# Optimization experiments

Measured on AMD Instinct MI355X. Metric: run time of the kernel, lower is better.

The kernel has to match this reference:

```python
import jax, jax.numpy as jnp
import numpy as np

B, D, L = 16, 256, 200
T = 1000   # max_frame_length
K = 3      # kernel_size
DW, DC = 4, 2


def setup_inputs() -> dict:
    key = jax.random.key(0)
    ks = jax.random.split(key, 16)
    plen = jax.random.randint(ks[0], (B,), 150, L + 1)
    pm = jnp.arange(L)[None, :] < plen[:, None]              # (B,L) True=valid
    phoneme_mask = pm[:, None, :]                            # (B,1,L)
    durations = jax.random.uniform(ks[1], (B, L), minval=1.0, maxval=8.0) * pm
    phoneme = jax.random.normal(ks[2], (B, D, L), dtype=jnp.float32)
    s = 0.05
    params = {
        'Wpw': jax.random.normal(ks[3], (D, D)) * s, 'bpw': jnp.zeros((D,)),
        'Cw': jax.random.normal(ks[4], (8, D, K)) * s, 'cbw': jnp.zeros((8,)),
        'Mw': jax.random.normal(ks[5], (10, DW)) * s, 'mbw': jnp.zeros((DW,)),
        'Lw': jax.random.normal(ks[6], (DW * D, D)) * s, 'lbw': jnp.zeros((D,)),
        'Wpc': jax.random.normal(ks[7], (D, D)) * s, 'bpc': jnp.zeros((D,)),
        'Cc': jax.random.normal(ks[8], (8, D, K)) * s, 'cbc': jnp.zeros((8,)),
        'Mc': jax.random.normal(ks[9], (10, DC)) * s, 'mbc': jnp.zeros((DC,)),
        'Lc': jax.random.normal(ks[10], (DW * DC, D)) * s, 'lbc': jnp.zeros((D,)),
        'Wo': jax.random.normal(ks[11], (D, 2 * D)) * s, 'bo': jnp.zeros((2 * D,)),
    }
    return {'durations': durations, 'phoneme': phoneme, 'phoneme_mask': phoneme_mask, **params}


def _conv_swish(x, W1, b1, Ck, cb, pm):
    # 1x1 conv (proj) then kernel-K 'same' conv then SiLU; mask padded phones
    h = jnp.einsum('od,bdl->bol', W1, x) + b1[None, :, None]
    h = jax.lax.conv_general_dilated(h, Ck, (1,), 'SAME',
                                     dimension_numbers=('NCH', 'OIH', 'NCH')) + cb[None, :, None]
    h = jax.nn.silu(h)
    h = jnp.where(pm[:, None, :], h, 0.0)
    return h.transpose(0, 2, 1)  # (B, L, 8)


def _mlp(S, E, h, M, mb):
    # concat start/end boundary scalars with per-phone conv features -> (B,T,L,10)
    feat = jnp.concatenate([S[..., None], E[..., None],
                            jnp.broadcast_to(h[:, None], (B, T, L, 8))], axis=-1)
    return jax.nn.silu(feat @ M + mb)


def _forward(durations, phoneme, phoneme_mask, Wpw, bpw, Cw, cbw, Mw, mbw, Lw, lbw,
             Wpc, bpc, Cc, cbc, Mc, mbc, Lc, lbc, Wo, bo):
    pm = phoneme_mask[:, 0, :]                                          # (B,L)
    frame_lengths = jnp.clip(jnp.round(durations.sum(-1)).astype(jnp.int32), 0, T)
    frame_mask = jnp.arange(T)[None, :] < frame_lengths[:, None]        # (B,T)
    attn_mask = frame_mask[:, :, None] & pm[:, None, :]                 # (B,T,L)
    sd = jnp.cumsum(durations, axis=-1)                                 # (B,L)
    sk = sd - durations
    t = jnp.arange(1, T + 1, dtype=durations.dtype)
    S = jnp.where(attn_mask, t[None, :, None] - sk[:, None, :], 0.0)    # (B,T,L)
    E = jnp.where(attn_mask, (sd - sk)[:, None, :], 0.0)                # (B,T,L)

    h_w = _conv_swish(phoneme, Wpw, bpw, Cw, cbw, pm)
    w = _mlp(S, E, h_w, Mw, mbw)                                        # (B,T,L,DW)
    w = jnp.where(pm[:, None, :, None], w, -jnp.inf)
    w = jax.nn.softmax(w, axis=2)                                       # softmax over phones
    w = jnp.where(frame_mask[:, :, None, None], w, 0.0)

    h_c = _conv_swish(phoneme, Wpc, bpc, Cc, cbc, pm)
    c = _mlp(S, E, h_c, Mc, mbc)                                        # (B,T,L,DC)

    wh = jnp.einsum('btlq,bdl->btqd', w, phoneme).reshape(B, T, DW * D) @ Lw + lbw
    wc = jnp.einsum('btlq,btlp->btqp', w, c).reshape(B, T, DW * DC) @ Lc + lbc
    whc = jnp.where(frame_mask[..., None], wh + wc, 0.0)                # (B,T,D)
    out = (whc @ Wo + bo).transpose(0, 2, 1)                            # (B,2D,T)
    return out, frame_mask, frame_lengths, w.transpose(0, 3, 1, 2)


def reference(durations, phoneme, phoneme_mask, Wpw, bpw, Cw, cbw, Mw, mbw, Lw, lbw,
              Wpc, bpc, Cc, cbc, Mc, mbc, Lc, lbc, Wo, bo):
    out, frame_mask, frame_lengths, w = _forward(
        durations, phoneme, phoneme_mask, Wpw, bpw, Cw, cbw, Mw, mbw, Lw, lbw,
        Wpc, bpc, Cc, cbc, Mc, mbc, Lc, lbc, Wo, bo)
    mean, log_std = jnp.split(out, 2, axis=1)                           # (B,D,T) each
    return (mean, log_std, frame_mask, frame_lengths, w)
```

## Files before the change

kernel.cpp:

```cpp
#include <hip/hip_runtime.h>
#include <hip/hip_bf16.h>
#include <math.h>

#define NB 16
#define ND 256
#define NL 200
#define NT 1000

typedef unsigned short ushort_t;
typedef __bf16 bf16x8 __attribute__((ext_vector_type(8)));
typedef float f32x4 __attribute__((ext_vector_type(4)));

#define OFF_PHT   0u
#define OFF_WCS   1000000u
#define OFF_SK    4966400u
#define OFF_EW    4969600u
#define OFF_EC    4975744u
#define OFF_BW2   4981888u
#define OFF_BC2   4981912u
#define OFF_FL    4981936u
#define OFF_WG    4981952u
#define OFF_GT    11535552u
#define OFF_WOT   15221952u
#define OFF_BASE  15287488u
#define OFF_PHTB  15320256u
#define OFF_LWT   15844544u

__device__ __forceinline__ float silu_f(float x){ return x / (1.f + __expf(-x)); }
__device__ __forceinline__ ushort_t f2bf(float x){
  __hip_bfloat16 h = __float2bfloat16(x);
  return *(ushort_t*)&h;
}

__global__ __launch_bounds__(256) void k_stage1(
    const float* __restrict__ dur, const float* __restrict__ ph,
    const float* __restrict__ Wp_w, const float* __restrict__ C_w, const float* __restrict__ bp_w,
    const float* __restrict__ Wp_c, const float* __restrict__ C_c, const float* __restrict__ bp_c,
    const float* __restrict__ Wo, const float* __restrict__ Lw,
    float* __restrict__ sk_ws, int* __restrict__ fl_ws,
    float* __restrict__ o_fm, float* __restrict__ o_fl,
    float* __restrict__ Ew, float* __restrict__ Ec,
    float* __restrict__ bw2, float* __restrict__ bc2,
    ushort_t* __restrict__ WoT, ushort_t* __restrict__ LwT,
    float* __restrict__ phT, ushort_t* __restrict__ phTb)
{
  int bid = blockIdx.x, tid = threadIdx.x;
  if (bid < 16){
    int b = bid;
    __shared__ float sdur[NL];
    __shared__ float ssk[NL];
    __shared__ int sfl;
    if (tid < NL) sdur[tid] = dur[b*NL + tid];
    __syncthreads();
    if (tid == 0){
      float run = 0.f;
      for (int l = 0; l < NL; ++l){ ssk[l] = run; run += sdur[l]; }
      int fl = (int)rintf(run);
      fl = fl < 0 ? 0 : (fl > NT ? NT : fl);
      sfl = fl; fl_ws[b] = fl; o_fl[b] = (float)fl;
    }
    __syncthreads();
    if (tid < NL) sk_ws[b*NL + tid] = ssk[tid];
    for (int t = tid; t < NT; t += 256) o_fm[b*NT + t] = (t < sfl) ? 1.f : 0.f;
  } else if (bid < 1600){
    int sbid = bid - 16;
    if (sbid < 48){
      int gid = sbid*256 + tid;
      int branch = gid / 6144;
      int r = gid % 6144;
      int d = r & 255;
      int ock = r >> 8;
      int oc = ock / 3, k = ock % 3;
      const float* Wp = branch ? Wp_c : Wp_w;
      const float* C  = branch ? C_c  : C_w;
      float acc = 0.f;
      for (int i = 0; i < ND; ++i) acc += C[(oc*ND + i)*3 + k] * Wp[i*ND + d];
      (branch ? Ec : Ew)[r] = acc;
      if (d == 0){
        const float* bp = branch ? bp_c : bp_w;
        float bb = 0.f;
        for (int i = 0; i < ND; ++i) bb += C[(oc*ND + i)*3 + k] * bp[i];
        (branch ? bc2 : bw2)[ock] = bb;
      }
    } else {
      int gid = (sbid - 48)*256 + tid;
      if (gid < 131072){
        int n = gid >> 8, k = gid & 255;
        WoT[gid] = f2bf(Wo[(size_t)k*512 + n]);
      } else {
        int r = gid - 131072;
        int d = r & 255;
        int qn = r >> 8;
        int q = qn >> 8, n = qn & 255;
        LwT[r] = f2bf(Lw[((size_t)q*256 + d)*256 + n]);
      }
    }
  } else {
    int r = bid - 1600;
    int xb = r & 7, yb = (r >> 3) & 7, b = r >> 6;
    int l0 = xb*32, d0 = yb*32;
    int tx = tid & 31, ty = tid >> 5;
    __shared__ float tile[32][33];
    #pragma unroll
    for (int i = 0; i < 4; ++i){
      int d = d0 + ty + i*8, l = l0 + tx;
      tile[ty + i*8][tx] = (l < NL) ? ph[((size_t)b*ND + d)*NL + l] : 0.f;
    }
    __syncthreads();
    #pragma unroll
    for (int i = 0; i < 4; ++i){
      int l = l0 + ty + i*8, d = d0 + tx;
      float v = tile[tx][ty + i*8];
      if (l < NL) phT[((size_t)b*NL + l)*ND + d] = v;
      phTb[((size_t)b*256 + l)*ND + d] = f2bf(v);
    }
  }
}

__global__ __launch_bounds__(256) void k_stage2(
    const float* __restrict__ phT,
    const float* __restrict__ dur, const float* __restrict__ sk_ws,
    const float* __restrict__ Ew, const float* __restrict__ Ec,
    const float* __restrict__ bw2, const float* __restrict__ bc2,
    const float* __restrict__ cbw, const float* __restrict__ cbc,
    const float* __restrict__ Mw, const float* __restrict__ mbw,
    const float* __restrict__ Mc, const float* __restrict__ mbc,
    float4* __restrict__ base,
    const ushort_t* __restrict__ LwT, const ushort_t* __restrict__ phTb,
    ushort_t* __restrict__ Gt)
{
  __shared__ __align__(16) unsigned char smem[128*136*2];
  int bid = blockIdx.x, tid = threadIdx.x;
  if (bid < 256){
    int b = bid >> 4, x = bid & 15;
    if (x >= 13){
      int l0 = 208 + (x - 13)*16;
      if (tid < 32)
        base[((size_t)(b*256 + l0 + (tid >> 1)))*2 + (tid & 1)] = make_float4(0,0,0,0);
      return;
    }
    float (*sh)[17] = (float (*)[17])smem;
    int lu = tid >> 4, u = tid & 15;
    int l = x*16 + lu;
    float h = 0.f;
    if (l < NL){
      int branch = u >> 3, oc = u & 7;
      const float* E  = branch ? Ec  : Ew;
      const float* b2 = branch ? bc2 : bw2;
      float val = (branch ? cbc : cbw)[oc];
      #pragma unroll
      for (int k = 0; k < 3; ++k){
        int ll = l + k - 1;
        if (ll < 0 || ll >= NL) continue;
        float acc = b2[oc*3 + k];
        const float4* Er = (const float4*)(E + (oc*3 + k)*ND);
        const float4* pr = (const float4*)(phT + ((size_t)b*NL + ll)*ND);
        #pragma unroll 8
        for (int d = 0; d < 64; ++d){
          float4 e = Er[d], p = pr[d];
          acc += e.x*p.x + e.y*p.y + e.z*p.z + e.w*p.w;
        }
        val += acc;
      }
      float pm = (dur[b*NL + l] > 0.5f) ? 1.f : 0.f;
      h = silu_f(val) * pm;
    }
    sh[lu][u] = h;
    __syncthreads();
    if (tid < 16){
      int ll = x*16 + tid;
      float4 o0 = make_float4(0,0,0,0);
      float4 o1 = make_float4(0,0,0,0);
      if (ll < NL){
        float dl  = dur[b*NL + ll];
        float pm  = (dl > 0.5f) ? 1.f : 0.f;
        float skl = sk_ws[b*NL + ll];
        float c1[4], c2[2];
        #pragma unroll
        for (int q = 0; q < 4; ++q) c1[q] = mbw[q] + dl*Mw[4 + q] - skl*Mw[q];
        #pragma unroll
        for (int p = 0; p < 2; ++p) c2[p] = mbc[p] + dl*Mc[2 + p] - skl*Mc[p];
        #pragma unroll
        for (int j = 0; j < 8; ++j){
          float hwv = sh[tid][j], hcv = sh[tid][8 + j];
          #pragma unroll
          for (int q = 0; q < 4; ++q) c1[q] += hwv*Mw[(2 + j)*4 + q];
          #pragma unroll
          for (int p = 0; p < 2; ++p) c2[p] += hcv*Mc[(2 + j)*2 + p];
        }
        o0 = make_float4(c1[0], c1[1], c1[2], c1[3]);
        o1 = make_float4(c2[0], c2[1], pm, 0.f);
      }
      base[((size_t)(b*256 + ll))*2 + 0] = o0;
      base[((size_t)(b*256 + ll))*2 + 1] = o1;
    }
  } else {
    int r = bid - 256;
    int xb = r & 1, yb = (r >> 1) & 1, bq = r >> 2;
    int b = bq >> 2, q = bq & 3;
    int m0 = yb * 128;
    int n0 = xb * 128;
    int lane = tid & 63, wave = tid >> 6;
    int wm = wave >> 1, wn = wave & 1;
    int col = lane & 15, kg4 = lane >> 4;
    f32x4 acc[4][4] = {};
    for (int kt = 0; kt < 8; ++kt){
      int k0 = kt*32;
      bf16x8 afr[4], bfr[4];
      #pragma unroll
      for (int i = 0; i < 4; ++i)
        afr[i] = *(const bf16x8*)(LwT + ((size_t)(q*256 + m0 + wm*64 + i*16 + col))*256 + k0 + kg4*8);
      #pragma unroll
      for (int j = 0; j < 4; ++j)
        bfr[j] = *(const bf16x8*)(phTb + ((size_t)(b*256 + n0 + wn*64 + j*16 + col))*256 + k0 + kg4*8);
      #pragma unroll
      for (int i = 0; i < 4; ++i)
        #pragma unroll
        for (int j = 0; j < 4; ++j)
          acc[i][j] = __builtin_amdgcn_mfma_f32_16x16x32_bf16(afr[i], bfr[j], acc[i][j], 0, 0, 0);
    }
    ushort_t (*st2)[136] = (ushort_t (*)[136])smem;
    int rq = lane >> 4;
    #pragma unroll
    for (int i = 0; i < 4; ++i){
      #pragma unroll
      for (int rr = 0; rr < 4; ++rr){
        int rl = wm*64 + i*16 + rq*4 + rr;
        #pragma unroll
        for (int j = 0; j < 4; ++j){
          int cl = wn*64 + j*16 + col;
          st2[rl][cl] = f2bf(acc[i][j][rr]);
        }
      }
    }
    __syncthreads();
    #pragma unroll
    for (int rep = 0; rep < 8; ++rep){
      int row = rep*16 + (tid >> 4);
      int ch  = tid & 15;
      int l   = n0 + ch*8;
      if (l < NL){
        int n = m0 + row;
        *(uint4*)(Gt + ((size_t)(b*ND + n))*800 + q*NL + l) = *(const uint4*)&st2[row][ch*8];
      }
    }
  }
}

__global__ __launch_bounds__(256) void k_softmax(
    const float4* __restrict__ base,
    const int* __restrict__ fl_ws,
    const float* __restrict__ Mw, const float* __restrict__ Mc,
    float* __restrict__ wout,
    ushort_t* __restrict__ wG,
    float* __restrict__ wcs_g)
{
  int lane = threadIdx.x & 63, wave = threadIdx.x >> 6;
  int wid = blockIdx.x*4 + wave;
  int b = wid >> 10, t = wid & 1023;
  int fl = fl_ws[b];
  ushort_t* wrow = wG + ((size_t)(b << 10) + t)*800;

  if (t >= fl){
    uint4 z16; z16.x = z16.y = z16.z = z16.w = 0u;
    for (int k = lane; k < 100; k += 64)
      *(uint4*)&wrow[k*8] = z16;
    if (lane < 8) wcs_g[((size_t)(b << 10) + t)*8 + lane] = 0.f;
    if (t < NT && lane < 50){
      float4 z4 = make_float4(0,0,0,0);
      #pragma unroll
      for (int q = 0; q < 4; ++q)
        *(float4*)&wout[(((size_t)(b*4 + q))*NT + t)*NL + lane*4] = z4;
    }
    return;
  }

  int l0 = lane*4;
  bool lv = (l0 < NL);
  float b0a[4][4], b1x[4], b1y[4], pmv[4];
  #pragma unroll
  for (int e = 0; e < 4; ++e){
    float4 v0 = make_float4(0,0,0,0), v1 = make_float4(0,0,0,0);
    if (lv){
      v0 = base[((size_t)(b*256 + l0 + e))*2 + 0];
      v1 = base[((size_t)(b*256 + l0 + e))*2 + 1];
    }
    b0a[e][0] = v0.x; b0a[e][1] = v0.y; b0a[e][2] = v0.z; b0a[e][3] = v0.w;
    b1x[e] = v1.x; b1y[e] = v1.y; pmv[e] = v1.z;
  }
  float tf = (float)(t + 1);

  float z[4][4], mx[4] = {-INFINITY, -INFINITY, -INFINITY, -INFINITY};
  #pragma unroll
  for (int e = 0; e < 4; ++e){
    #pragma unroll
    for (int q = 0; q < 4; ++q){
      float sv = silu_f(b0a[e][q] + tf*Mw[q]);
      float zv = (pmv[e] > 0.f) ? sv : -INFINITY;
      z[e][q] = zv;
      mx[q] = fmaxf(mx[q], zv);
    }
  }
  #pragma unroll
  for (int q = 0; q < 4; ++q){
    float v = mx[q];
    #pragma unroll
    for (int off = 32; off; off >>= 1) v = fmaxf(v, __shfl_xor(v, off));
    mx[q] = v;
  }
  float s4[4] = {0,0,0,0};
  #pragma unroll
  for (int e = 0; e < 4; ++e){
    #pragma unroll
    for (int q = 0; q < 4; ++q){
      float ev = (pmv[e] > 0.f) ? __expf(z[e][q] - mx[q]) : 0.f;
      z[e][q] = ev;
      s4[q] += ev;
    }
  }
  #pragma unroll
  for (int q = 0; q < 4; ++q){
    float v = s4[q];
    #pragma unroll
    for (int off = 32; off; off >>= 1) v += __shfl_xor(v, off);
    s4[q] = 1.f / v;
  }
  float cv[4][2];
  #pragma unroll
  for (int e = 0; e < 4; ++e){
    cv[e][0] = silu_f(b1x[e] + tf*Mc[0]);
    cv[e][1] = silu_f(b1y[e] + tf*Mc[1]);
  }
  float wc[8] = {0,0,0,0,0,0,0,0};
  #pragma unroll
  for (int q = 0; q < 4; ++q){
    float w0 = z[0][q]*s4[q];
    float w1 = z[1][q]*s4[q];
    float w2 = z[2][q]*s4[q];
    float w3 = z[3][q]*s4[q];
    if (lv){
      *(float4*)&wout[(((size_t)(b*4 + q))*NT + t)*NL + l0] =
          make_float4(w0, w1, w2, w3);
      uint2 pk;
      pk.x = (unsigned)f2bf(w0) | ((unsigned)f2bf(w1) << 16);
      pk.y = (unsigned)f2bf(w2) | ((unsigned)f2bf(w3) << 16);
      *(uint2*)&wrow[q*NL + l0] = pk;
    }
    wc[q*2 + 0] += w0*cv[0][0] + w1*cv[1][0] + w2*cv[2][0] + w3*cv[3][0];
    wc[q*2 + 1] += w0*cv[0][1] + w1*cv[1][1] + w2*cv[2][1] + w3*cv[3][1];
  }
  #pragma unroll
  for (int x = 0; x < 8; ++x){
    float v = wc[x];
    #pragma unroll
    for (int off = 32; off; off >>= 1) v += __shfl_xor(v, off);
    wc[x] = v;
  }
  if (lane == 0){
    #pragma unroll
    for (int x = 0; x < 8; ++x) wcs_g[((size_t)(b << 10) + t)*8 + x] = wc[x];
  }
}

#define TT 64
__global__ __launch_bounds__(1024, 4) void k_wv2(
    const int* __restrict__ fl_ws,
    const ushort_t* __restrict__ wG,
    const ushort_t* __restrict__ Gt,
    const float* __restrict__ wcs_g,
    const float* __restrict__ Lc,
    const float* __restrict__ lbc,
    const float* __restrict__ lbw,
    const ushort_t* __restrict__ WoT,
    const float* __restrict__ bo,
    float* __restrict__ o_mean, float* __restrict__ o_lstd)
{
  __shared__ ushort_t stc[TT][264];
  __shared__ float wcs_l[TT][8];
  int b = blockIdx.x;
  int m0 = blockIdx.y * TT;
  int tid = threadIdx.x, lane = tid & 63, wave = tid >> 6;
  int col = lane & 15, kg4 = lane >> 4;
  int fl = fl_ws[b];

  if (fl <= m0){
    for (int idx = tid; idx < 512*16; idx += 1024){
      int s = idx >> 4, j = idx & 15;
      int t0 = m0 + j*4;
      if (t0 + 3 < NT){
        float v = bo[s];
        float4 v4 = make_float4(v, v, v, v);
        if (s < ND) *(float4*)&o_mean[((size_t)b*ND + s)*NT + t0] = v4;
        else        *(float4*)&o_lstd[((size_t)b*ND + (s - ND))*NT + t0] = v4;
      }
    }
    return;
  }

  if (tid < 512){
    int tl = tid >> 3, u = tid & 7;
    wcs_l[tl][u] = wcs_g[((size_t)(b << 10) + m0 + tl)*8 + u];
  }

  f32x4 acc[4] = {};
  const ushort_t* Gb = Gt + (size_t)b*ND*800;
  const ushort_t* Wb = wG + ((size_t)(b << 10) + m0)*800;
  for (int kt = 0; kt < 25; ++kt){
    int k0 = kt*32;
    bf16x8 afr[4], bfr;
    #pragma unroll
    for (int i = 0; i < 4; ++i)
      afr[i] = *(const bf16x8*)(Wb + ((size_t)(i*16 + col))*800 + k0 + kg4*8);
    bfr = *(const bf16x8*)(Gb + ((size_t)(wave*16 + col))*800 + k0 + kg4*8);
    #pragma unroll
    for (int i = 0; i < 4; ++i)
      acc[i] = __builtin_amdgcn_mfma_f32_16x16x32_bf16(afr[i], bfr, acc[i], 0, 0, 0);
  }
  __syncthreads();

  {
    int rq = lane >> 4;
    int n = wave*16 + col;
    float lbn = lbc[n], lbwn = lbw[n];
    float lcn[8];
    #pragma unroll
    for (int u = 0; u < 8; ++u) lcn[u] = Lc[u*ND + n];
    #pragma unroll
    for (int i = 0; i < 4; ++i){
      #pragma unroll
      for (int r = 0; r < 4; ++r){
        int tl = i*16 + rq*4 + r;
        int t = m0 + tl;
        if (t < NT){
          float f = (t < fl) ? 1.f : 0.f;
          float vcv = lbn
            + wcs_l[tl][0]*lcn[0] + wcs_l[tl][1]*lcn[1]
            + wcs_l[tl][2]*lcn[2] + wcs_l[tl][3]*lcn[3]
            + wcs_l[tl][4]*lcn[4] + wcs_l[tl][5]*lcn[5]
            + wcs_l[tl][6]*lcn[6] + wcs_l[tl][7]*lcn[7];
          stc[tl][n] = f2bf(f * (acc[i][r] + lbwn + vcv));
        }
      }
    }
  }
  __syncthreads();

  {
    f32x4 acc2[2][4] = {};
    for (int kt = 0; kt < 8; ++kt){
      int k0 = kt*32;
      bf16x8 afr[2], bfr[4];
      #pragma unroll
      for (int j = 0; j < 4; ++j)
        bfr[j] = *(const bf16x8*)(&stc[j*16 + col][k0 + kg4*8]);
      #pragma unroll
      for (int i = 0; i < 2; ++i)
        afr[i] = *(const bf16x8*)(WoT + ((size_t)(wave*32 + i*16 + col))*ND + k0 + kg4*8);
      #pragma unroll
      for (int i = 0; i < 2; ++i)
        #pragma unroll
        for (int j = 0; j < 4; ++j)
          acc2[i][j] = __builtin_amdgcn_mfma_f32_16x16x32_bf16(afr[i], bfr[j], acc2[i][j], 0, 0, 0);
    }
    int rq = lane >> 4;
    #pragma unroll
    for (int i = 0; i < 2; ++i){
      #pragma unroll
      for (int r = 0; r < 4; ++r){
        int s = wave*32 + i*16 + rq*4 + r;
        float bov = bo[s];
        #pragma unroll
        for (int j = 0; j < 4; ++j){
          int t = m0 + j*16 + col;
          if (t < NT){
            float v = acc2[i][j][r] + bov;
            if (s < ND) o_mean[((size_t)b*ND + s)*NT + t] = v;
            else        o_lstd[((size_t)b*ND + (s - ND))*NT + t] = v;
          }
        }
      }
    }
  }
}

extern "C" void kernel_launch(void* const* d_in, const int* in_sizes, int n_in,
                              void* d_out, int out_size, void* d_ws, size_t ws_size,
                              hipStream_t stream)
{
  const float* dur = (const float*)d_in[0];
  const float* ph  = (const float*)d_in[1];
  const float* Wpw = (const float*)d_in[3];
  const float* bpw = (const float*)d_in[4];
  const float* Cw  = (const float*)d_in[5];
  const float* cbw = (const float*)d_in[6];
  const float* Mw  = (const float*)d_in[7];
  const float* mbw = (const float*)d_in[8];
  const float* Lw  = (const float*)d_in[9];
  const float* lbw = (const float*)d_in[10];
  const float* Wpc = (const float*)d_in[11];
  const float* bpc = (const float*)d_in[12];
  const float* Cc  = (const float*)d_in[13];
  const float* cbc = (const float*)d_in[14];
  const float* Mc  = (const float*)d_in[15];
  const float* mbc = (const float*)d_in[16];
  const float* Lc  = (const float*)d_in[17];
  const float* lbc = (const float*)d_in[18];
  const float* Wo  = (const float*)d_in[19];
  const float* bo  = (const float*)d_in[20];

  float* out    = (float*)d_out;
  float* o_mean = out;
  float* o_lstd = out + (size_t)NB*ND*NT;
  float* o_fm   = o_lstd + (size_t)NB*ND*NT;
  float* o_fl   = o_fm + NB*NT;
  float* o_w    = o_fl + NB;

  float* ws   = (float*)d_ws;
  float* phT  = ws + OFF_PHT;
  float* wcsg = ws + OFF_WCS;
  float* sk   = ws + OFF_SK;
  float* Ew   = ws + OFF_EW;
  float* Ec   = ws + OFF_EC;
  float* bw2  = ws + OFF_BW2;
  float* bc2  = ws + OFF_BC2;
  int*   fl   = (int*)(ws + OFF_FL);
  ushort_t* wG   = (ushort_t*)(ws + OFF_WG);
  ushort_t* Gt   = (ushort_t*)(ws + OFF_GT);
  ushort_t* WoT  = (ushort_t*)(ws + OFF_WOT);
  float4*   base = (float4*)(ws + OFF_BASE);
  ushort_t* phTb = (ushort_t*)(ws + OFF_PHTB);
  ushort_t* LwT  = (ushort_t*)(ws + OFF_LWT);

  k_stage1<<<2624, 256, 0, stream>>>(dur, ph, Wpw, Cw, bpw, Wpc, Cc, bpc, Wo, Lw,
                                     sk, fl, o_fm, o_fl, Ew, Ec, bw2, bc2,
                                     WoT, LwT, phT, phTb);
  k_stage2<<<512, 256, 0, stream>>>(phT, dur, sk, Ew, Ec, bw2, bc2, cbw, cbc,
                                    Mw, mbw, Mc, mbc, base, LwT, phTb, Gt);
  k_softmax<<<4096, 256, 0, stream>>>(base, fl, Mw, Mc, o_w, wG, wcsg);
  {
    dim3 g(NB, 16);
    k_wv2<<<g, 1024, 0, stream>>>(fl, wG, Gt, wcsg, Lc, lbc, lbw,
                                  WoT, bo, o_mean, o_lstd);
  }
}
```

Measured before the change: 260.2 us.

## Fuse softmax attention weights into the weighted-value GEMM kernel via LDS

New measurement: 250.9 us. -3.6%, faster.

```diff
diff --git a/kernel.cpp b/kernel.cpp
--- a/kernel.cpp
+++ b/kernel.cpp
@@ -12,14 +12,12 @@
 typedef float f32x4 __attribute__((ext_vector_type(4)));
 
 #define OFF_PHT   0u
-#define OFF_WCS   1000000u
 #define OFF_SK    4966400u
 #define OFF_EW    4969600u
 #define OFF_EC    4975744u
 #define OFF_BW2   4981888u
 #define OFF_BC2   4981912u
 #define OFF_FL    4981936u
-#define OFF_WG    4981952u
 #define OFF_GT    11535552u
 #define OFF_WOT   15221952u
 #define OFF_BASE  15287488u
@@ -247,36 +245,71 @@
   }
 }
 
-__global__ __launch_bounds__(256) void k_softmax(
+#define AP 808
+#define TT 48
+__global__ __launch_bounds__(512, 4) void k_wv_fused(
     const float4* __restrict__ base,
     const int* __restrict__ fl_ws,
     const float* __restrict__ Mw, const float* __restrict__ Mc,
+    const ushort_t* __restrict__ Gt,
+    const float* __restrict__ Lc,
+    const float* __restrict__ lbc,
+    const float* __restrict__ lbw,
+    const ushort_t* __restrict__ WoT,
+    const float* __restrict__ bo,
     float* __restrict__ wout,
-    ushort_t* __restrict__ wG,
-    float* __restrict__ wcs_g)
+    float* __restrict__ o_mean, float* __restrict__ o_lstd)
 {
-  int lane = threadIdx.x & 63, wave = threadIdx.x >> 6;
-  int wid = blockIdx.x*4 + wave;
-  int b = wid >> 10, t = wid & 1023;
+  __shared__ ushort_t As[TT*AP];
+  __shared__ float    wcs[TT][8];
+  int b = blockIdx.x;
+  int m0 = blockIdx.y * TT;
+  int tid = threadIdx.x, lane = tid & 63, wave = tid >> 6;
+  int col = lane & 15, kg4 = lane >> 4;
   int fl = fl_ws[b];
-  ushort_t* wrow = wG + ((size_t)(b << 10) + t)*800;
-
-  if (t >= fl){
-    uint4 z16; z16.x = z16.y = z16.z = z16.w = 0u;
-    for (int k = lane; k < 100; k += 64)
-      *(uint4*)&wrow[k*8] = z16;
-    if (lane < 8) wcs_g[((size_t)(b << 10) + t)*8 + lane] = 0.f;
-    if (t < NT && lane < 50){
-      float4 z4 = make_float4(0,0,0,0);
-      #pragma unroll
-      for (int q = 0; q < 4; ++q)
-        *(float4*)&wout[(((size_t)(b*4 + q))*NT + t)*NL + lane*4] = z4;
+
+  if (fl <= m0){
+    for (int idx = tid; idx < TT*4*50; idx += 512){
+      int tl = idx / 200;
+      int rqs = idx - tl*200;
+      int q = rqs / 50, seg = rqs - q*50;
+      int t = m0 + tl;
+      if (t < NT)
+        *(float4*)&wout[(((size_t)(b*4 + q))*NT + t)*NL + seg*4] = make_float4(0,0,0,0);
+    }
+    for (int idx = tid; idx < 512*12; idx += 512){
+      int s = idx / 12, j = idx - s*12;
+      int t0 = m0 + j*4;
+      if (t0 + 3 < NT){
+        float v = bo[s];
+        float4 v4 = make_float4(v, v, v, v);
+        if (s < ND) *(float4*)&o_mean[((size_t)b*ND + s)*NT + t0] = v4;
+        else        *(float4*)&o_lstd[((size_t)b*ND + (s - ND))*NT + t0] = v4;
+      }
     }
     return;
   }
 
   int l0 = lane*4;
   bool lv = (l0 < NL);
+
+  #pragma unroll
+  for (int s = 0; s < 6; ++s){
+    int tl = wave*6 + s, t = m0 + tl;
+    if (t < fl) continue;
+    for (int k = l0; k < 800; k += 256){
+      uint2 zz2; zz2.x = 0u; zz2.y = 0u;
+      *(uint2*)&As[tl*AP + k] = zz2;
+    }
+    if (lane < 8) wcs[tl][lane] = 0.f;
+    if (t < NT && lv){
+      float4 z4 = make_float4(0,0,0,0);
+      #pragma unroll
+      for (int q = 0; q < 4; ++q)
+        *(float4*)&wout[(((size_t)(b*4 + q))*NT + t)*NL + l0] = z4;
+    }
+  }
+
   float b0a[4][4], b1x[4], b1y[4], pmv[4];
   #pragma unroll
   for (int e = 0; e < 4; ++e){
@@ -288,157 +321,136 @@
     b0a[e][0] = v0.x; b0a[e][1] = v0.y; b0a[e][2] = v0.z; b0a[e][3] = v0.w;
     b1x[e] = v1.x; b1y[e] = v1.y; pmv[e] = v1.z;
   }
-  float tf = (float)(t + 1);
-
-  float z[4][4], mx[4] = {-INFINITY, -INFINITY, -INFINITY, -INFINITY};
-  #pragma unroll
-  for (int e = 0; e < 4; ++e){
+  float mwq[4] = {Mw[0], Mw[1], Mw[2], Mw[3]};
+  float mcp[2] = {Mc[0], Mc[1]};
+
+  for (int s = 0; s < 6; ++s){
+    int tl = wave*6 + s;
+    int t = m0 + tl;
+    if (t >= fl) break;
+    float tf = (float)(t + 1);
+
+    float z[4][4], mx[4] = {-INFINITY, -INFINITY, -INFINITY, -INFINITY};
+    #pragma unroll
+    for (int e = 0; e < 4; ++e){
+      #pragma unroll
+      for (int q = 0; q < 4; ++q){
+        float sv = silu_f(b0a[e][q] + tf*mwq[q]);
+        float zv = (pmv[e] > 0.f) ? sv : -INFINITY;
+        z[e][q] = zv;
+        mx[q] = fmaxf(mx[q], zv);
+      }
+    }
     #pragma unroll
     for (int q = 0; q < 4; ++q){
-      float sv = silu_f(b0a[e][q] + tf*Mw[q]);
-      float zv = (pmv[e] > 0.f) ? sv : -INFINITY;
-      z[e][q] = zv;
-      mx[q] = fmaxf(mx[q], zv);
-    }
-  }
-  #pragma unroll
-  for (int q = 0; q < 4; ++q){
-    float v = mx[q];
-    #pragma unroll
-    for (int off = 32; off; off >>= 1) v = fmaxf(v, __shfl_xor(v, off));
-    mx[q] = v;
-  }
-  float s4[4] = {0,0,0,0};
-  #pragma unroll
-  for (int e = 0; e < 4; ++e){
+      float v = mx[q];
+      #pragma unroll
+      for (int off = 32; off; off >>= 1) v = fmaxf(v, __shfl_xor(v, off));
+      mx[q] = v;
+    }
+    float s4[4] = {0,0,0,0};
+    #pragma unroll
+    for (int e = 0; e < 4; ++e){
+      #pragma unroll
+      for (int q = 0; q < 4; ++q){
+        float ev = (pmv[e] > 0.f) ? __expf(z[e][q] - mx[q]) : 0.f;
+        z[e][q] = ev;
+        s4[q] += ev;
+      }
+    }
     #pragma unroll
     for (int q = 0; q < 4; ++q){
-      float ev = (pmv[e] > 0.f) ? __expf(z[e][q] - mx[q]) : 0.f;
-      z[e][q] = ev;
-      s4[q] += ev;
-    }
-  }
-  #pragma unroll
-  for (int q = 0; q < 4; ++q){
-    float v = s4[q];
-    #pragma unroll
-    for (int off = 32; off; off >>= 1) v += __shfl_xor(v, off);
-    s4[q] = 1.f / v;
-  }
-  float cv[4][2];
-  #pragma unroll
-  for (int e = 0; e < 4; ++e){
-    cv[e][0] = silu_f(b1x[e] + tf*Mc[0]);
-    cv[e][1] = silu_f(b1y[e] + tf*Mc[1]);
-  }
-  float wc[8] = {0,0,0,0,0,0,0,0};
-  #pragma unroll
-  for (int q = 0; q < 4; ++q){
-    float w0 = z[0][q]*s4[q];
-    float w1 = z[1][q]*s4[q];
-    float w2 = z[2][q]*s4[q];
-    float w3 = z[3][q]*s4[q];
-    if (lv){
-      *(float4*)&wout[(((size_t)(b*4 + q))*NT + t)*NL + l0] =
-          make_float4(w0, w1, w2, w3);
-      uint2 pk;
-      pk.x = (unsigned)f2bf(w0) | ((unsigned)f2bf(w1) << 16);
-      pk.y = (unsigned)f2bf(w2) | ((unsigned)f2bf(w3) << 16);
-      *(uint2*)&wrow[q*NL + l0] = pk;
-    }
-    wc[q*2 + 0] += w0*cv[0][0] + w1*cv[1][0] + w2*cv[2][0] + w3*cv[3][0];
-    wc[q*2 + 1] += w0*cv[0][1] + w1*cv[1][1] + w2*cv[2][1] + w3*cv[3][1];
-  }
-  #pragma unroll
-  for (int x = 0; x < 8; ++x){
-    float v = wc[x];
-    #pragma unroll
-    for (int off = 32; off; off >>= 1) v += __shfl_xor(v, off);
-    wc[x] = v;
-  }
-  if (lane == 0){
-    #pragma unroll
-    for (int x = 0; x < 8; ++x) wcs_g[((size_t)(b << 10) + t)*8 + x] = wc[x];
-  }
-}
-
-#define TT 64
-__global__ __launch_bounds__(1024, 4) void k_wv2(
-    const int* __restrict__ fl_ws,
-    const ushort_t* __restrict__ wG,
-    const ushort_t* __restrict__ Gt,
-    const float* __restrict__ wcs_g,
-    const float* __restrict__ Lc,
-    const float* __restrict__ lbc,
-    const float* __restrict__ lbw,
-    const ushort_t* __restrict__ WoT,
-    const float* __restrict__ bo,
-    float* __restrict__ o_mean, float* __restrict__ o_lstd)
-{
-  __shared__ ushort_t stc[TT][264];
-  __shared__ float wcs_l[TT][8];
-  int b = blockIdx.x;
-  int m0 = blockIdx.y * TT;
-  int tid = threadIdx.x, lane = tid & 63, wave = tid >> 6;
-  int col = lane & 15, kg4 = lane >> 4;
-  int fl = fl_ws[b];
-
-  if (fl <= m0){
-    for (int idx = tid; idx < 512*16; idx += 1024){
-      int s = idx >> 4, j = idx & 15;
-      int t0 = m0 + j*4;
-      if (t0 + 3 < NT){
-        float v = bo[s];
-        float4 v4 = make_float4(v, v, v, v);
-        if (s < ND) *(float4*)&o_mean[((size_t)b*ND + s)*NT + t0] = v4;
-        else        *(float4*)&o_lstd[((size_t)b*ND + (s - ND))*NT + t0] = v4;
-      }
-    }
-    return;
-  }
-
-  if (tid < 512){
-    int tl = tid >> 3, u = tid & 7;
-    wcs_l[tl][u] = wcs_g[((size_t)(b << 10) + m0 + tl)*8 + u];
-  }
-
-  f32x4 acc[4] = {};
+      float v = s4[q];
+      #pragma unroll
+      for (int off = 32; off; off >>= 1) v += __shfl_xor(v, off);
+      s4[q] = 1.f / v;
+    }
+    float cv[4][2];
+    #pragma unroll
+    for (int e = 0; e < 4; ++e){
+      cv[e][0] = silu_f(b1x[e] + tf*mcp[0]);
+      cv[e][1] = silu_f(b1y[e] + tf*mcp[1]);
+    }
+    float wc[8] = {0,0,0,0,0,0,0,0};
+    #pragma unroll
+    for (int q = 0; q < 4; ++q){
+      float w0 = z[0][q]*s4[q];
+      float w1 = z[1][q]*s4[q];
+      float w2 = z[2][q]*s4[q];
+      float w3 = z[3][q]*s4[q];
+      if (lv){
+        *(float4*)&wout[(((size_t)(b*4 + q))*NT + t)*NL + l0] =
+            make_float4(w0, w1, w2, w3);
+        uint2 pk;
+        pk.x = (unsigned)f2bf(w0) | ((unsigned)f2bf(w1) << 16);
+        pk.y = (unsigned)f2bf(w2) | ((unsigned)f2bf(w3) << 16);
+        *(uint2*)&As[tl*AP + q*NL + l0] = pk;
+      }
+      wc[q*2 + 0] += w0*cv[0][0] + w1*cv[1][0] + w2*cv[2][0] + w3*cv[3][0];
+      wc[q*2 + 1] += w0*cv[0][1] + w1*cv[1][1] + w2*cv[2][1] + w3*cv[3][1];
+    }
+    #pragma unroll
+    for (int x = 0; x < 8; ++x){
+      float v = wc[x];
+      #pragma unroll
+      for (int off = 32; off; off >>= 1) v += __shfl_xor(v, off);
+      wc[x] = v;
+    }
+    if (lane == 0){
+      #pragma unroll
+      for (int x = 0; x < 8; ++x) wcs[tl][x] = wc[x];
+    }
+  }
+  __syncthreads();
+
+  f32x4 acc[3][2] = {};
   const ushort_t* Gb = Gt + (size_t)b*ND*800;
-  const ushort_t* Wb = wG + ((size_t)(b << 10) + m0)*800;
   for (int kt = 0; kt < 25; ++kt){
     int k0 = kt*32;
-    bf16x8 afr[4], bfr;
-    #pragma unroll
-    for (int i = 0; i < 4; ++i)
-      afr[i] = *(const bf16x8*)(Wb + ((size_t)(i*16 + col))*800 + k0 + kg4*8);
-    bfr = *(const bf16x8*)(Gb + ((size_t)(wave*16 + col))*800 + k0 + kg4*8);
-    #pragma unroll
-    for (int i = 0; i < 4; ++i)
-      acc[i] = __builtin_amdgcn_mfma_f32_16x16x32_bf16(afr[i], bfr, acc[i], 0, 0, 0);
+    bf16x8 afr[3], bfr[2];
+    #pragma unroll
+    for (int i = 0; i < 3; ++i)
+      afr[i] = *(const bf16x8*)(&As[(i*16 + col)*AP + k0 + kg4*8]);
+    #pragma unroll
+    for (int j = 0; j < 2; ++j)
+      bfr[j] = *(const bf16x8*)(Gb + ((size_t)(wave*32 + j*16 + col))*800 + k0 + kg4*8);
+    #pragma unroll
+    for (int i = 0; i < 3; ++i)
+      #pragma unroll
+      for (int j = 0; j < 2; ++j)
+        acc[i][j] = __builtin_amdgcn_mfma_f32_16x16x32_bf16(afr[i], bfr[j], acc[i][j], 0, 0, 0);
   }
   __syncthreads();
 
+  ushort_t (*stc)[264] = (ushort_t (*)[264])As;
   {
     int rq = lane >> 4;
-    int n = wave*16 + col;
-    float lbn = lbc[n], lbwn = lbw[n];
-    float lcn[8];
-    #pragma unroll
-    for (int u = 0; u < 8; ++u) lcn[u] = Lc[u*ND + n];
-    #pragma unroll
-    for (int i = 0; i < 4; ++i){
+    float lcn[2][8], lbn[2], lbwn[2];
+    #pragma unroll
+    for (int j = 0; j < 2; ++j){
+      int n = wave*32 + j*16 + col;
+      lbn[j] = lbc[n]; lbwn[j] = lbw[n];
+      #pragma unroll
+      for (int u = 0; u < 8; ++u) lcn[j][u] = Lc[u*ND + n];
+    }
+    #pragma unroll
+    for (int i = 0; i < 3; ++i){
       #pragma unroll
       for (int r = 0; r < 4; ++r){
         int tl = i*16 + rq*4 + r;
         int t = m0 + tl;
         if (t < NT){
           float f = (t < fl) ? 1.f : 0.f;
-          float vcv = lbn
-            + wcs_l[tl][0]*lcn[0] + wcs_l[tl][1]*lcn[1]
-            + wcs_l[tl][2]*lcn[2] + wcs_l[tl][3]*lcn[3]
-            + wcs_l[tl][4]*lcn[4] + wcs_l[tl][5]*lcn[5]
-            + wcs_l[tl][6]*lcn[6] + wcs_l[tl][7]*lcn[7];
-          stc[tl][n] = f2bf(f * (acc[i][r] + lbwn + vcv));
+          #pragma unroll
+          for (int j = 0; j < 2; ++j){
+            float vcv = lbn[j]
+              + wcs[tl][0]*lcn[j][0] + wcs[tl][1]*lcn[j][1]
+              + wcs[tl][2]*lcn[j][2] + wcs[tl][3]*lcn[j][3]
+              + wcs[tl][4]*lcn[j][4] + wcs[tl][5]*lcn[j][5]
+              + wcs[tl][6]*lcn[j][6] + wcs[tl][7]*lcn[j][7];
+            int n = wave*32 + j*16 + col;
+            stc[tl][n] = f2bf(f * (acc[i][j][r] + lbwn[j] + vcv));
+          }
         }
       }
     }
@@ -446,31 +458,31 @@
   __syncthreads();
 
   {
-    f32x4 acc2[2][4] = {};
+    f32x4 acc2[4][3] = {};
     for (int kt = 0; kt < 8; ++kt){
       int k0 = kt*32;
-      bf16x8 afr[2], bfr[4];
-      #pragma unroll
-      for (int j = 0; j < 4; ++j)
+      bf16x8 afr[4], bfr[3];
+      #pragma unroll
+      for (int j = 0; j < 3; ++j)
         bfr[j] = *(const bf16x8*)(&stc[j*16 + col][k0 + kg4*8]);
       #pragma unroll
-      for (int i = 0; i < 2; ++i)
-        afr[i] = *(const bf16x8*)(WoT + ((size_t)(wave*32 + i*16 + col))*ND + k0 + kg4*8);
-      #pragma unroll
-      for (int i = 0; i < 2; ++i)
-        #pragma unroll
-        for (int j = 0; j < 4; ++j)
+      for (int i = 0; i < 4; ++i)
+        afr[i] = *(const bf16x8*)(WoT + ((size_t)(wave*64 + i*16 + col))*ND + k0 + kg4*8);
+      #pragma unroll
+      for (int i = 0; i < 4; ++i)
+        #pragma unroll
+        for (int j = 0; j < 3; ++j)
           acc2[i][j] = __builtin_amdgcn_mfma_f32_16x16x32_bf16(afr[i], bfr[j], acc2[i][j], 0, 0, 0);
     }
     int rq = lane >> 4;
     #pragma unroll
-    for (int i = 0; i < 2; ++i){
+    for (int i = 0; i < 4; ++i){
       #pragma unroll
       for (int r = 0; r < 4; ++r){
-        int s = wave*32 + i*16 + rq*4 + r;
+        int s = wave*64 + i*16 + rq*4 + r;
         float bov = bo[s];
         #pragma unroll
-        for (int j = 0; j < 4; ++j){
+        for (int j = 0; j < 3; ++j){
           int t = m0 + j*16 + col;
           if (t < NT){
             float v = acc2[i][j][r] + bov;
@@ -517,14 +529,12 @@
 
   float* ws   = (float*)d_ws;
   float* phT  = ws + OFF_PHT;
-  float* wcsg = ws + OFF_WCS;
   float* sk   = ws + OFF_SK;
   float* Ew   = ws + OFF_EW;
   float* Ec   = ws + OFF_EC;
   float* bw2  = ws + OFF_BW2;
   float* bc2  = ws + OFF_BC2;
   int*   fl   = (int*)(ws + OFF_FL);
-  ushort_t* wG   = (ushort_t*)(ws + OFF_WG);
   ushort_t* Gt   = (ushort_t*)(ws + OFF_GT);
   ushort_t* WoT  = (ushort_t*)(ws + OFF_WOT);
   float4*   base = (float4*)(ws + OFF_BASE);
@@ -536,10 +546,9 @@
                                      WoT, LwT, phT, phTb);
   k_stage2<<<512, 256, 0, stream>>>(phT, dur, sk, Ew, Ec, bw2, bc2, cbw, cbc,
                                     Mw, mbw, Mc, mbc, base, LwT, phTb, Gt);
-  k_softmax<<<4096, 256, 0, stream>>>(base, fl, Mw, Mc, o_w, wG, wcsg);
   {
-    dim3 g(NB, 16);
-    k_wv2<<<g, 1024, 0, stream>>>(fl, wG, Gt, wcsg, Lc, lbc, lbw,
-                                  WoT, bo, o_mean, o_lstd);
+    dim3 g(NB, 21);
+    k_wv_fused<<<g, 512, 0, stream>>>(base, fl, Mw, Mc, Gt, Lc, lbc, lbw,
+                                      WoT, bo, o_w, o_mean, o_lstd);
   }
 }
```
